# Optimization experiments

Hardware: AMD Instinct MI355X
Metric: run time of the kernel (lower is better)

## Reference

```python
import jax, jax.numpy as jnp
import numpy as np
import math

SUB = 0.8  # subset fraction (init kwarg)


def _capsule_weighted_average(x):
    # x: [B, I, O, D, H, W]; norm-weighted average over input caps (dim 1)
    n = jnp.linalg.norm(x, axis=3, keepdims=True)  # [B, I, O, 1, H, W]
    return (n * x).sum(axis=1) / n.sum(axis=1)      # [B, O, D, H, W]


def setup_inputs() -> dict:
    key = jax.random.key(0)
    # [B, input_caps, output_caps, pose_dim, H, W, kh, kw]
    x = jax.random.normal(key, (8, 32, 32, 8, 14, 14, 3, 3), dtype=jnp.float32)
    return {"x": x}


def reference(x):
    B, I, O, D, H, W = x.shape[:6]
    x = x.reshape(B, I, O, D, H, W, -1)             # flatten kernel positions -> K
    # norm-weighted average over the K kernel positions
    xn = jnp.linalg.norm(x, axis=3, keepdims=True)  # [B, I, O, 1, H, W, K]
    x = (xn * x).sum(axis=-1) / xn.sum(axis=-1)     # [B, I, O, D, H, W]

    v = _capsule_weighted_average(x)                # [B, O, D, H, W]

    # 'mse' metric: negative dot product between consensus v and each input capsule
    losses = -(v[:, None] * x).sum(axis=3)          # [B, I, O, H, W]
    subset_size = math.ceil(SUB * I)
    # kthvalue (k-th smallest) along input-caps dim
    thr = jnp.sort(losses, axis=1)[:, subset_size - 1:subset_size]  # [B, 1, O, H, W]
    choose = (losses <= thr).astype(x.dtype)[:, :, :, None]          # [B, I, O, 1, H, W]
    x = x * jax.lax.stop_gradient(choose)

    return _capsule_weighted_average(x)             # [B, O, D, H, W]
```

## Files before the change

kernel.cpp:

```cpp
#include <hip/hip_runtime.h>

#define B 8
#define I 32
#define O 32
#define D 8
#define H 14
#define W 14
#define K 9
#define WK (W*K)
#define DSTRIDE (H*W*K)
#define OSTRIDE (D*H*W*K)
#define ISTRIDE (O*D*H*W*K)
#define BSTRIDE ((size_t)I*ISTRIDE)
#define SUBSET 26

__global__ __launch_bounds__(448) void caps_route_kernel(const float* __restrict__ x,
                                                         float* __restrict__ out) {
    const int bid = blockIdx.x;
    const int h = bid % H;
    const int o = (bid / H) % O;
    const int b = bid / (H * O);
    const int t = threadIdx.x;
    const int i = t / W;
    const int w = t - i * W;

    __shared__ float ys[I][D][W];
    __shared__ float ns_s[I][W];
    __shared__ float ls_s[I][W];
    __shared__ float vsh[D][W];
    __shared__ float thr_s[W];

    const float* xp = x + (size_t)b * BSTRIDE + (size_t)i * ISTRIDE
                        + (size_t)o * OSTRIDE + (size_t)h * WK + (size_t)w * K;

    float xv[D][K];
    #pragma unroll
    for (int d = 0; d < D; ++d) {
        #pragma unroll
        for (int k = 0; k < K; ++k) {
            xv[d][k] = xp[d * DSTRIDE + k];
        }
    }

    float nk[K];
    float den = 0.f;
    #pragma unroll
    for (int k = 0; k < K; ++k) {
        float s = 0.f;
        #pragma unroll
        for (int d = 0; d < D; ++d) { float v = xv[d][k]; s += v * v; }
        nk[k] = sqrtf(s);
        den += nk[k];
    }
    const float inv_den = 1.f / den;

    float y[D];
    float s2 = 0.f;
    #pragma unroll
    for (int d = 0; d < D; ++d) {
        float num = 0.f;
        #pragma unroll
        for (int k = 0; k < K; ++k) num += nk[k] * xv[d][k];
        y[d] = num * inv_den;
        ys[i][d][w] = y[d];
        s2 += y[d] * y[d];
    }
    const float nsv = sqrtf(s2);
    ns_s[i][w] = nsv;
    __syncthreads();

    if (t < D * W) {
        const int d = t / W, w2 = t - (t / W) * W;
        float num = 0.f, dn = 0.f;
        #pragma unroll
        for (int j = 0; j < I; ++j) {
            float nv = ns_s[j][w2];
            num += nv * ys[j][d][w2];
            dn += nv;
        }
        vsh[d][w2] = num / dn;
    }
    __syncthreads();

    float lv = 0.f;
    #pragma unroll
    for (int d = 0; d < D; ++d) lv += vsh[d][w] * y[d];
    lv = -lv;
    ls_s[i][w] = lv;
    __syncthreads();

    int rank = 0;
    #pragma unroll
    for (int j = 0; j < I; ++j) {
        float lj = ls_s[j][w];
        rank += (lj < lv || (lj == lv && j < i)) ? 1 : 0;
    }
    if (rank == SUBSET - 1) thr_s[w] = lv;
    __syncthreads();

    if (t < D * W) {
        const int d = t / W, w2 = t - (t / W) * W;
        const float tw = thr_s[w2];
        float num = 0.f, dn = 0.f;
        #pragma unroll
        for (int j = 0; j < I; ++j) {
            float m  = (ls_s[j][w2] <= tw) ? 1.f : 0.f;
            float nv = m * ns_s[j][w2];
            num += nv * ys[j][d][w2];
            dn  += nv;
        }
        out[(((size_t)b * O + o) * D + d) * (H * W) + h * W + w2] = num / dn;
    }
}

extern "C" void kernel_launch(void* const* d_in, const int* in_sizes, int n_in,
                              void* d_out, int out_size, void* d_ws, size_t ws_size,
                              hipStream_t stream) {
    const float* x = (const float*)d_in[0];
    float* out = (float*)d_out;
    dim3 grid(B * O * H);
    dim3 block(I * W);
    caps_route_kernel<<<grid, block, 0, stream>>>(x, out);
}
```

Baseline: 605.8 us.

## Split into coalesced K-reduction kernel and routing kernel via workspace

Splits the fused kernel in two. The first kernel loads each contiguous (b,i,o) slab of x into shared memory with float4 loads, computes the kernel-position norms and the weighted averages, and writes a compact intermediate to the workspace in a layout grouped by (b,o,h). The second kernel reads that intermediate with vectorized loads and runs the consensus, rank-threshold and masked-average steps as before. This replaces the strided, poorly coalesced 9-element per-thread reads of the 1.1 GB input with fully coalesced streaming. The cost is an extra launch and an intermediate buffer write and read, which is small next to the input.

```diff
diff --git a/kernel.cpp b/kernel.cpp
--- a/kernel.cpp
+++ b/kernel.cpp
@@ -13,60 +13,93 @@
 #define ISTRIDE (O*D*H*W*K)
 #define BSTRIDE ((size_t)I*ISTRIDE)
 #define SUBSET 26
+#define SLAB (D*H*WK)
+#define SLAB4 (SLAB/4)
+#define YS_BLOCK (I*W*D)
 
-__global__ __launch_bounds__(448) void caps_route_kernel(const float* __restrict__ x,
-                                                         float* __restrict__ out) {
+__global__ __launch_bounds__(256) void k_reduce(const float* __restrict__ x,
+                                                float* __restrict__ ys) {
+    const int bid = blockIdx.x;
+    const int o = bid % O;
+    const int i = (bid / O) % I;
+    const int b = bid / (O * I);
+    const int t = threadIdx.x;
+
+    __shared__ float xs[SLAB];
+    __shared__ float nk[DSTRIDE];
+
+    const float4* src = (const float4*)(x + (size_t)b * BSTRIDE
+                                          + (size_t)i * ISTRIDE
+                                          + (size_t)o * OSTRIDE);
+    float4* xs4 = (float4*)xs;
+    #pragma unroll
+    for (int it = 0; it < 14; ++it) {
+        int idx = it * 256 + t;
+        if (idx < SLAB4) xs4[idx] = src[idx];
+    }
+    __syncthreads();
+
+    #pragma unroll
+    for (int it = 0; it < 7; ++it) {
+        int j = it * 256 + t;
+        if (j < DSTRIDE) {
+            float s = 0.f;
+            #pragma unroll
+            for (int d = 0; d < D; ++d) { float v = xs[d * DSTRIDE + j]; s += v * v; }
+            nk[j] = sqrtf(s);
+        }
+    }
+    __syncthreads();
+
+    if (t < H * W) {
+        const int h = t / W, w = t - (t / W) * W;
+        const int jb = h * WK + w * K;
+        float nkv[K];
+        float den = 0.f;
+        #pragma unroll
+        for (int k = 0; k < K; ++k) { nkv[k] = nk[jb + k]; den += nkv[k]; }
+        const float inv = 1.f / den;
+        float y[D];
+        #pragma unroll
+        for (int d = 0; d < D; ++d) {
+            float num = 0.f;
+            #pragma unroll
+            for (int k = 0; k < K; ++k) num += nkv[k] * xs[d * DSTRIDE + jb + k];
+            y[d] = num * inv;
+        }
+        float4* dst = (float4*)(ys + ((((size_t)(b * O + o) * H + h) * I + i) * W + w) * D);
+        dst[0] = make_float4(y[0], y[1], y[2], y[3]);
+        dst[1] = make_float4(y[4], y[5], y[6], y[7]);
+    }
+}
+
+__global__ __launch_bounds__(448) void k_route(const float* __restrict__ ys,
+                                               float* __restrict__ out) {
     const int bid = blockIdx.x;
     const int h = bid % H;
     const int o = (bid / H) % O;
     const int b = bid / (H * O);
     const int t = threadIdx.x;
-    const int i = t / W;
-    const int w = t - i * W;
+    const int i = t / W, w = t - (t / W) * W;
 
-    __shared__ float ys[I][D][W];
-    __shared__ float ns_s[I][W];
-    __shared__ float ls_s[I][W];
-    __shared__ float vsh[D][W];
+    __shared__ float ysl[YS_BLOCK];
+    __shared__ float ns_s[I * W];
+    __shared__ float ls_s[I * W];
+    __shared__ float vsh[D * W];
     __shared__ float thr_s[W];
 
-    const float* xp = x + (size_t)b * BSTRIDE + (size_t)i * ISTRIDE
-                        + (size_t)o * OSTRIDE + (size_t)h * WK + (size_t)w * K;
-
-    float xv[D][K];
-    #pragma unroll
-    for (int d = 0; d < D; ++d) {
-        #pragma unroll
-        for (int k = 0; k < K; ++k) {
-            xv[d][k] = xp[d * DSTRIDE + k];
-        }
-    }
-
-    float nk[K];
-    float den = 0.f;
-    #pragma unroll
-    for (int k = 0; k < K; ++k) {
-        float s = 0.f;
-        #pragma unroll
-        for (int d = 0; d < D; ++d) { float v = xv[d][k]; s += v * v; }
-        nk[k] = sqrtf(s);
-        den += nk[k];
-    }
-    const float inv_den = 1.f / den;
+    const float4* src = (const float4*)(ys + (size_t)bid * YS_BLOCK);
+    float4* ysl4 = (float4*)ysl;
+    ysl4[t] = src[t];
+    ysl4[t + 448] = src[t + 448];
+    __syncthreads();
 
     float y[D];
     float s2 = 0.f;
     #pragma unroll
-    for (int d = 0; d < D; ++d) {
-        float num = 0.f;
-        #pragma unroll
-        for (int k = 0; k < K; ++k) num += nk[k] * xv[d][k];
-        y[d] = num * inv_den;
-        ys[i][d][w] = y[d];
-        s2 += y[d] * y[d];
-    }
+    for (int d = 0; d < D; ++d) { y[d] = ysl[t * D + d]; s2 += y[d] * y[d]; }
     const float nsv = sqrtf(s2);
-    ns_s[i][w] = nsv;
+    ns_s[t] = nsv;
     __syncthreads();
 
     if (t < D * W) {
@@ -74,25 +107,25 @@
         float num = 0.f, dn = 0.f;
         #pragma unroll
         for (int j = 0; j < I; ++j) {
-            float nv = ns_s[j][w2];
-            num += nv * ys[j][d][w2];
+            float nv = ns_s[j * W + w2];
+            num += nv * ysl[(j * W + w2) * D + d];
             dn += nv;
         }
-        vsh[d][w2] = num / dn;
+        vsh[d * W + w2] = num / dn;
     }
     __syncthreads();
 
     float lv = 0.f;
     #pragma unroll
-    for (int d = 0; d < D; ++d) lv += vsh[d][w] * y[d];
+    for (int d = 0; d < D; ++d) lv += vsh[d * W + w] * y[d];
     lv = -lv;
-    ls_s[i][w] = lv;
+    ls_s[t] = lv;
     __syncthreads();
 
     int rank = 0;
     #pragma unroll
     for (int j = 0; j < I; ++j) {
-        float lj = ls_s[j][w];
+        float lj = ls_s[j * W + w];
         rank += (lj < lv || (lj == lv && j < i)) ? 1 : 0;
     }
     if (rank == SUBSET - 1) thr_s[w] = lv;
@@ -104,9 +137,10 @@
         float num = 0.f, dn = 0.f;
         #pragma unroll
         for (int j = 0; j < I; ++j) {
-            float m  = (ls_s[j][w2] <= tw) ? 1.f : 0.f;
-            float nv = m * ns_s[j][w2];
-            num += nv * ys[j][d][w2];
+            float ls = ls_s[j * W + w2];
+            float m  = (ls <= tw) ? 1.f : 0.f;
+            float nv = m * ns_s[j * W + w2];
+            num += nv * ysl[(j * W + w2) * D + d];
             dn  += nv;
         }
         out[(((size_t)b * O + o) * D + d) * (H * W) + h * W + w2] = num / dn;
@@ -118,7 +152,8 @@
                               hipStream_t stream) {
     const float* x = (const float*)d_in[0];
     float* out = (float*)d_out;
-    dim3 grid(B * O * H);
-    dim3 block(I * W);
-    caps_route_kernel<<<grid, block, 0, stream>>>(x, out);
+    float* ys = (float*)d_ws;
+
+    k_reduce<<<dim3(B * I * O), dim3(256), 0, stream>>>(x, ys);
+    k_route<<<dim3(B * O * H), dim3(448), 0, stream>>>(ys, out);
 }
```

Result: slower. 620.7 us (+2.5%).
